# Kernel optimization log

Hardware: AMD Instinct MI355X
Metric: run time of the kernel (lower is better)

The kernel has to match this reference:

```python
import jax, jax.numpy as jnp
import numpy as np

N = 100000          # nodes
E = 1600000         # edges
IN, H, E1, E2, K = 256, 128, 128, 128, 3


def setup_inputs() -> dict:
    key = jax.random.key(0)
    ks = jax.random.split(key, 8)
    s = 0.02
    return {
        "x": jax.random.normal(ks[0], (N, IN), dtype=jnp.float32),
        "edge_index": jax.random.randint(ks[1], (2, E), 0, N),
        "edge_weight": jax.random.uniform(ks[2], (E,), dtype=jnp.float32),
        "W1": jax.random.normal(ks[3], (IN, H), dtype=jnp.float32) * s,
        "b1": jnp.zeros((H,), jnp.float32),
        "cheb1_W": jax.random.normal(ks[4], (K, H, E1), dtype=jnp.float32) * s,
        "cheb1_b": jnp.zeros((E1,), jnp.float32),
        "cheb2_W": jax.random.normal(ks[5], (K, E1, E2), dtype=jnp.float32) * s,
        "cheb2_b": jnp.zeros((E2,), jnp.float32),
        "W2": jax.random.normal(ks[6], (E2, 2), dtype=jnp.float32) * s,
        "b2": jnp.zeros((2,), jnp.float32),
    }


def _cheb_conv(x, row, col, wn, Ws, b):
    """PyG ChebConv with sym normalization, lambda_max=2.
    Scaled Laplacian L_hat = L_sym - I = -D^{-1/2} A D^{-1/2} (zero diagonal),
    so L_hat @ v is a single gather/scale/scatter over edges.
    Tx_0 = x; Tx_1 = L_hat x; Tx_k = 2 L_hat Tx_{k-1} - Tx_{k-2}.
    """
    n = x.shape[0]

    def Lx(v):
        return jax.ops.segment_sum(-wn[:, None] * v[col], row, num_segments=n)

    Tx0 = x
    out = Tx0 @ Ws[0]
    Tx1 = Lx(Tx0)
    out = out + Tx1 @ Ws[1]
    for k in range(2, Ws.shape[0]):
        Tx2 = 2.0 * Lx(Tx1) - Tx0
        out = out + Tx2 @ Ws[k]
        Tx0, Tx1 = Tx1, Tx2
    return out + b


def reference(x, edge_index, edge_weight, W1, b1, cheb1_W, cheb1_b,
              cheb2_W, cheb2_b, W2, b2):
    row, col = edge_index[0], edge_index[1]
    n = x.shape[0]
    # symmetric normalization of edge weights (shared by both convs)
    deg = jax.ops.segment_sum(edge_weight, row, num_segments=n)
    safe = jnp.where(deg > 0, deg, 1.0)
    dinv = jnp.where(deg > 0, jax.lax.rsqrt(safe), 0.0)
    wn = dinv[row] * edge_weight * dinv[col]

    # dropout is identity in eval mode
    h = jax.nn.relu(x @ W1 + b1)
    h = jax.nn.relu(_cheb_conv(h, row, col, wn, cheb1_W, cheb1_b))
    h = jax.nn.relu(_cheb_conv(h, row, col, wn, cheb2_W, cheb2_b))
    logits = h @ W2 + b2
    return jax.nn.softmax(logits, axis=1)
```

## Files before the change

kernel.cpp:

```cpp
#include <hip/hip_runtime.h>
#include <hip/hip_bf16.h>
#include <stdint.h>

typedef __bf16 bf16_t;
typedef __bf16 bf16x8 __attribute__((ext_vector_type(8)));
typedef float f32x4 __attribute__((ext_vector_type(4)));
typedef float f32x2 __attribute__((ext_vector_type(2)));
typedef float floatv4 __attribute__((ext_vector_type(4)));

static __device__ __forceinline__ void gload16(const void* g, void* l){
  __builtin_amdgcn_global_load_lds((const __attribute__((address_space(1))) void*)g,
                                   (__attribute__((address_space(3))) void*)l, 16, 0, 0);
}
static __device__ __forceinline__ void acc4_fp8(float* a, unsigned w, float wt){
  f32x2 lo, hi;
  unsigned wh = w >> 16;
  asm("v_cvt_pk_f32_fp8 %0, %1" : "=v"(lo) : "v"(w));
  asm("v_cvt_pk_f32_fp8 %0, %1" : "=v"(hi) : "v"(wh));
  a[0] += wt*lo[0]; a[1] += wt*lo[1]; a[2] += wt*hi[0]; a[3] += wt*hi[1];
}
static __device__ __forceinline__ void dec4_fp8(float* d, unsigned w){
  f32x2 lo, hi;
  unsigned wh = w >> 16;
  asm("v_cvt_pk_f32_fp8 %0, %1" : "=v"(lo) : "v"(w));
  asm("v_cvt_pk_f32_fp8 %0, %1" : "=v"(hi) : "v"(wh));
  d[0] = lo[0]; d[1] = lo[1]; d[2] = hi[0]; d[3] = hi[1];
}
static __device__ __forceinline__ unsigned cvt2fp8(float a, float b){
  unsigned r;
  asm("v_cvt_pk_fp8_f32 %0, %1, %2" : "=v"(r) : "v"(a), "v"(b));
  return r & 0xffffu;
}
static __device__ __forceinline__ uint8_t cvt1fp8(float a){
  unsigned r;
  asm("v_cvt_pk_fp8_f32 %0, %1, %1" : "=v"(r) : "v"(a));
  return (uint8_t)r;
}
static __device__ __forceinline__ unsigned packEdge(int col, float w_pos){
  unsigned b = __float_as_uint(w_pos) + 0x8000u;
  return ((b >> 16) << 17) | (unsigned)col;
}
static __device__ __forceinline__ float edgeWpos(unsigned u){
  return __uint_as_float((u >> 17) << 16);
}
static __device__ __forceinline__ float edgeWneg(unsigned u){
  return __uint_as_float(0x80000000u | ((u >> 17) << 16));
}

constexpr int NN = 100000;
constexpr int NE = 1600000;
constexpr int NB_G  = (NN + 127)/128;
constexpr int NBIN = (NN + 127)/128;
constexpr int EPB  = 4096;
constexpr int NBB  = (NE + EPB - 1)/EPB;
constexpr int MAXBE = 3072;
constexpr int NB_TW8 = (2*3*128*128)/256;

__global__ __launch_bounds__(256) void k_scanbins(const int* __restrict__ bincnt,
                                                  int* __restrict__ binptr,
                                                  int* __restrict__ rowptr){
  __shared__ int s[256];
  int t = threadIdx.x;
  int b0 = t*4;
  int c[4]; int tot = 0;
  #pragma unroll
  for (int j = 0; j < 4; ++j){
    int b = b0 + j;
    c[j] = (b < NBIN) ? bincnt[b] : 0;
    tot += c[j];
  }
  s[t] = tot;
  __syncthreads();
  for (int off = 1; off < 256; off <<= 1){
    int v = (t >= off) ? s[t - off] : 0;
    __syncthreads();
    s[t] += v;
    __syncthreads();
  }
  int ex = s[t] - tot;
  #pragma unroll
  for (int j = 0; j < 4; ++j){
    int b = b0 + j;
    if (b < NBIN) binptr[b] = ex;
    ex += c[j];
  }
  if (t == 255){ binptr[NBIN] = ex; rowptr[NN] = ex; }
}

__global__ __launch_bounds__(256) void k_binB(const int* __restrict__ row,
                                              const int* __restrict__ col,
                                              const float* __restrict__ w,
                                              const int* __restrict__ binptr,
                                              const int* __restrict__ blockbase,
                                              int2* __restrict__ temp){
  __shared__ int h[NBIN];
  for (int b = threadIdx.x; b < NBIN; b += 256) h[b] = 0;
  __syncthreads();
  int base = blockIdx.x * EPB;
  for (int k = 0; k < EPB; k += 256){
    int i = base + k + threadIdx.x;
    if (i < NE){
      int r = row[i];
      int b = r >> 7;
      int rank = atomicAdd(&h[b], 1);
      int pos = binptr[b] + blockbase[blockIdx.x * NBIN + b] + rank;
      temp[pos] = make_int2(col[i] | ((r & 127) << 17), __float_as_int(w[i]));
    }
  }
}

__global__ __launch_bounds__(256) void k_binC(const int2* __restrict__ temp,
                                              const int* __restrict__ binptr,
                                              unsigned* __restrict__ ec,
                                              int* __restrict__ rowptr,
                                              float* __restrict__ dinv, int n){
  __shared__ int2 sbuf[MAXBE];
  __shared__ int cnt[128];
  __shared__ int scan[128];
  __shared__ int estart[128];
  const int b = blockIdx.x;
  const int e0 = binptr[b];
  int nb = binptr[b+1] - e0; if (nb > MAXBE) nb = MAXBE;
  const int t = threadIdx.x;
  if (t < 128) cnt[t] = 0;
  __syncthreads();
  for (int k = t; k < nb; k += 256)
    atomicAdd(&cnt[(temp[e0+k].x >> 17) & 127], 1);
  __syncthreads();
  if (t < 128) scan[t] = cnt[t];
  __syncthreads();
  for (int off = 1; off < 128; off <<= 1){
    int v = (t < 128 && t >= off) ? scan[t - off] : 0;
    __syncthreads();
    if (t < 128) scan[t] += v;
    __syncthreads();
  }
  if (t < 128){ estart[t] = scan[t] - cnt[t]; cnt[t] = 0; }
  __syncthreads();
  for (int k = t; k < nb; k += 256){
    int2 q = temp[e0+k];
    int rl = (q.x >> 17) & 127;
    int rank = atomicAdd(&cnt[rl], 1);
    sbuf[estart[rl] + rank] = q;
  }
  __syncthreads();
  for (int k = t; k < nb; k += 256){
    int2 q = sbuf[k];
    ec[e0 + k] = packEdge(q.x & 0x1FFFF, __int_as_float(q.y));
  }
  if (t < 128){
    int gid = b*128 + t;
    if (gid < n){
      rowptr[gid] = e0 + estart[t];
      float s = 0.f;
      int s0 = estart[t], c = cnt[t];
      for (int j = 0; j < c; ++j) s += __int_as_float(sbuf[s0+j].y);
      dinv[gid] = (s > 0.f) ? rsqrtf(s) : 0.f;
    }
  }
}

__global__ __launch_bounds__(256) void k_norm(unsigned* __restrict__ ec,
                                              const int* __restrict__ rowptr,
                                              const float* __restrict__ dinv, int n){
  int node = blockIdx.x*4 + (threadIdx.x >> 6);
  if (node >= n) return;
  int lane = threadIdx.x & 63;
  int e0 = rowptr[node], e1 = rowptr[node+1];
  float dr = dinv[node];
  for (int e = e0 + lane; e < e1; e += 64){
    unsigned u = ec[e];
    int c = u & 0x1FFFF;
    float wn = dr * edgeWpos(u) * dinv[c];
    ec[e] = packEdge(c, wn);
  }
}

__global__ void k_transw1(const float* __restrict__ W1, bf16_t* __restrict__ Wt1){
  int idx = blockIdx.x*256 + threadIdx.x;
  int c = idx >> 14, r = (idx >> 7) & 127, j = idx & 127;
  Wt1[(c << 14) + (j << 7) + r] = (bf16_t)W1[idx];
}

__global__ __launch_bounds__(256) void k_gemm1_fused(
    const float* __restrict__ x, const bf16_t* __restrict__ Wt, const float* __restrict__ bias,
    uint8_t* __restrict__ out8, int M,
    const int* __restrict__ row, int* __restrict__ bincnt, int* __restrict__ blockbase,
    const float* __restrict__ c1W, const float* __restrict__ c2W,
    uint8_t* __restrict__ W8c1, uint8_t* __restrict__ W8c2)
{
  __shared__ uint8_t lds[2][16384];
  __shared__ int hA[NBIN];
  const int tid = threadIdx.x;

  if (blockIdx.x >= NB_G + NBB){
    int base = (blockIdx.x - NB_G - NBB)*256 + tid;
    int m = base / 49152;
    int local = base - m*49152;
    const float* src = m ? c2W : c1W;
    uint8_t* dst = m ? W8c2 : W8c1;
    int c = local >> 14, r = (local >> 7) & 127, j = local & 127;
    dst[(c << 14) + (j << 7) + r] = cvt1fp8(src[local]);
    return;
  }
  if (blockIdx.x >= NB_G){
    int bb = blockIdx.x - NB_G;
    for (int b = tid; b < NBIN; b += 256) hA[b] = 0;
    __syncthreads();
    int base = bb * EPB;
    for (int k = 0; k < EPB; k += 256){
      int i = base + k + tid;
      if (i < NE) atomicAdd(&hA[row[i] >> 7], 1);
    }
    __syncthreads();
    for (int b = tid; b < NBIN; b += 256){
      int c = hA[b];
      blockbase[bb * NBIN + b] = c ? atomicAdd(&bincnt[b], c) : 0;
    }
    return;
  }

  const int wave = tid >> 6, lane = tid & 63;
  const int wm = wave >> 1, wn = wave & 1;
  const int l15 = lane & 15, lq = lane >> 4;
  const int blockRow = blockIdx.x * 128;
  const int strow = tid >> 3;
  const int scell = tid & 7;

  f32x4 acc[4][4];
  #pragma unroll
  for (int a = 0; a < 4; ++a)
    #pragma unroll
    for (int b = 0; b < 4; ++b) acc[a][b] = f32x4{0.f,0.f,0.f,0.f};

  #pragma unroll
  for (int j = 0; j < 4; ++j){
    int r = j*32 + strow;
    int gr = blockRow + r; if (gr > M-1) gr = M-1;
    gload16((const char*)x + (size_t)gr*1024 + ((scell ^ (r&7)) << 4),
            &lds[0][j*4096 + tid*16]);
  }

  #pragma unroll
  for (int s = 0; s < 8; ++s){
    if (s < 7){
      #pragma unroll
      for (int j = 0; j < 4; ++j){
        int r = j*32 + strow;
        int gr = blockRow + r; if (gr > M-1) gr = M-1;
        gload16((const char*)x + (size_t)gr*1024 + (s+1)*128 + ((scell ^ (r&7)) << 4),
                &lds[(s+1)&1][j*4096 + tid*16]);
      }
    }
    __syncthreads();
    const uint8_t* buf = lds[s&1];
    bf16x8 af[4], bfr[4];
    #pragma unroll
    for (int fm = 0; fm < 4; ++fm){
      int r = wm*64 + fm*16 + l15;
      floatv4 v0 = *(const floatv4*)(buf + r*128 + (((lq*2    ) ^ (r&7)) << 4));
      floatv4 v1 = *(const floatv4*)(buf + r*128 + (((lq*2 + 1) ^ (r&7)) << 4));
      bf16x8 t;
      t[0]=(bf16_t)v0[0]; t[1]=(bf16_t)v0[1]; t[2]=(bf16_t)v0[2]; t[3]=(bf16_t)v0[3];
      t[4]=(bf16_t)v1[0]; t[5]=(bf16_t)v1[1]; t[6]=(bf16_t)v1[2]; t[7]=(bf16_t)v1[3];
      af[fm] = t;
    }
    #pragma unroll
    for (int fn = 0; fn < 4; ++fn)
      bfr[fn] = *(const bf16x8*)(Wt + ((size_t)(((s>>2) << 7) + wn*64 + fn*16 + l15) << 7) + (s&3)*32 + lq*8);
    #pragma unroll
    for (int fm = 0; fm < 4; ++fm)
      #pragma unroll
      for (int fn = 0; fn < 4; ++fn)
        acc[fm][fn] = __builtin_amdgcn_mfma_f32_16x16x32_bf16(af[fm], bfr[fn], acc[fm][fn], 0, 0, 0);
    __syncthreads();
  }
  #pragma unroll
  for (int fm = 0; fm < 4; ++fm){
    #pragma unroll
    for (int j = 0; j < 4; ++j){
      int growo = blockRow + wm*64 + fm*16 + lq*4 + j;
      if (growo < M){
        #pragma unroll
        for (int fn = 0; fn < 4; ++fn){
          int c = wn*64 + fn*16 + l15;
          float v = fmaxf(acc[fm][fn][j] + bias[c], 0.f);
          out8[((size_t)growo << 7) + c] = cvt1fp8(v);
        }
      }
    }
  }
}

__global__ __launch_bounds__(256) void k_gemm8(
    const uint8_t* __restrict__ a0, const uint8_t* __restrict__ a1, const uint8_t* __restrict__ a2,
    const uint8_t* __restrict__ Wt8, const float* __restrict__ bias,
    uint8_t* __restrict__ out8,
    const float* __restrict__ W2h, const float* __restrict__ b2h, float* __restrict__ outh,
    int M)
{
  __shared__ uint8_t lds[2][8192];
  __shared__ float logits[128][2][2];
  const int tid = threadIdx.x;
  const int wave = tid >> 6, lane = tid & 63;
  const int wm = wave >> 1, wn = wave & 1;
  const int l15 = lane & 15, lq = lane >> 4;
  const int blockRow = blockIdx.x * 128;

  f32x4 acc[4][4];
  #pragma unroll
  for (int a = 0; a < 4; ++a)
    #pragma unroll
    for (int b = 0; b < 4; ++b) acc[a][b] = f32x4{0.f,0.f,0.f,0.f};

  #pragma unroll
  for (int j = 0; j < 2; ++j){
    int flat = j*256 + tid;
    int r = flat >> 2, cell = flat & 3;
    int gr = blockRow + r; if (gr > M-1) gr = M-1;
    gload16(a0 + (size_t)gr*128 + ((cell ^ ((r>>1)&3)) << 4), &lds[0][flat << 4]);
  }

  #pragma unroll
  for (int s = 0; s < 6; ++s){
    if (s < 5){
      const int sn = s + 1;
      const uint8_t* srcn = (sn>>1) == 0 ? a0 : ((sn>>1) == 1 ? a1 : a2);
      #pragma unroll
      for (int j = 0; j < 2; ++j){
        int flat = j*256 + tid;
        int r = flat >> 2, cell = flat & 3;
        int gr = blockRow + r; if (gr > M-1) gr = M-1;
        gload16(srcn + (size_t)gr*128 + (sn&1)*64 + ((cell ^ ((r>>1)&3)) << 4),
                &lds[sn&1][flat << 4]);
      }
    }
    __syncthreads();
    const uint8_t* buf = lds[s&1];
    #pragma unroll
    for (int kk32 = 0; kk32 < 2; ++kk32){
      long af[4], bfr[4];
      #pragma unroll
      for (int fm = 0; fm < 4; ++fm){
        int r = wm*64 + fm*16 + l15;
        int cell = kk32*2 + (lq >> 1);
        af[fm] = *(const long*)(buf + r*64 + ((cell ^ ((r>>1)&3)) << 4) + (lq & 1)*8);
      }
      #pragma unroll
      for (int fn = 0; fn < 4; ++fn)
        bfr[fn] = *(const long*)(Wt8 + ((size_t)(((s>>1) << 7) + wn*64 + fn*16 + l15) << 7)
                                 + (s&1)*64 + kk32*32 + lq*8);
      #pragma unroll
      for (int fm = 0; fm < 4; ++fm)
        #pragma unroll
        for (int fn = 0; fn < 4; ++fn)
          acc[fm][fn] = __builtin_amdgcn_mfma_f32_16x16x32_fp8_fp8(af[fm], bfr[fn], acc[fm][fn], 0, 0, 0);
    }
    __syncthreads();
  }

  if (outh){
    float w2l[8];
    #pragma unroll
    for (int fn = 0; fn < 4; ++fn){
      int c = wn*64 + fn*16 + l15;
      w2l[fn*2]   = W2h[c*2];
      w2l[fn*2+1] = W2h[c*2+1];
    }
    #pragma unroll
    for (int fm = 0; fm < 4; ++fm){
      #pragma unroll
      for (int j = 0; j < 4; ++j){
        int r = wm*64 + fm*16 + lq*4 + j;
        float p0 = 0.f, p1 = 0.f;
        #pragma unroll
        for (int fn = 0; fn < 4; ++fn){
          float v = fmaxf(acc[fm][fn][j] + bias[wn*64 + fn*16 + l15], 0.f);
          p0 += v*w2l[fn*2];
          p1 += v*w2l[fn*2+1];
        }
        #pragma unroll
        for (int m = 1; m < 16; m <<= 1){
          p0 += __shfl_xor(p0, m, 64);
          p1 += __shfl_xor(p1, m, 64);
        }
        if (l15 == 0){
          logits[r][wn][0] = p0;
          logits[r][wn][1] = p1;
        }
      }
    }
    __syncthreads();
    if (tid < 128){
      int node = blockRow + tid;
      if (node < M){
        float l0 = logits[tid][0][0] + logits[tid][1][0] + b2h[0];
        float l1 = logits[tid][0][1] + logits[tid][1][1] + b2h[1];
        float mx = fmaxf(l0, l1);
        float e0 = __expf(l0 - mx), e1 = __expf(l1 - mx);
        float inv = 1.f / (e0 + e1);
        *(float2*)(outh + (size_t)node*2) = make_float2(e0*inv, e1*inv);
      }
    }
  } else {
    #pragma unroll
    for (int fm = 0; fm < 4; ++fm){
      #pragma unroll
      for (int j = 0; j < 4; ++j){
        int growo = blockRow + wm*64 + fm*16 + lq*4 + j;
        if (growo < M){
          #pragma unroll
          for (int fn = 0; fn < 4; ++fn){
            int c = wn*64 + fn*16 + l15;
            float v = fmaxf(acc[fm][fn][j] + bias[c], 0.f);
            out8[((size_t)growo << 7) + c] = cvt1fp8(v);
          }
        }
      }
    }
  }
}

__global__ __launch_bounds__(256) void k_spmm8(
    const int* __restrict__ rowptr, const unsigned* __restrict__ ec,
    const uint8_t* __restrict__ V8, const uint8_t* __restrict__ sub8, float alpha,
    uint8_t* __restrict__ out8, int n)
{
  const int lane = threadIdx.x & 63;
  const int wave = threadIdx.x >> 6;
  const int g = lane >> 4;
  const int s = lane & 15;
  const int node = blockIdx.x*16 + wave*4 + g;
  if (node >= n) return;

  int e = rowptr[node];
  const int e1 = rowptr[node+1];
  const int fb = s << 3;

  float acc[8] = {0.f,0.f,0.f,0.f,0.f,0.f,0.f,0.f};

  for (; e + 8 <= e1; e += 8){
    unsigned u0 = ec[e],   u1 = ec[e+1], u2 = ec[e+2], u3 = ec[e+3];
    unsigned u4 = ec[e+4], u5 = ec[e+5], u6 = ec[e+6], u7 = ec[e+7];
    uint2 p0 = *(const uint2*)(V8 + (((size_t)(u0 & 0x1FFFF)) << 7) + fb);
    uint2 p1 = *(const uint2*)(V8 + (((size_t)(u1 & 0x1FFFF)) << 7) + fb);
    uint2 p2 = *(const uint2*)(V8 + (((size_t)(u2 & 0x1FFFF)) << 7) + fb);
    uint2 p3 = *(const uint2*)(V8 + (((size_t)(u3 & 0x1FFFF)) << 7) + fb);
    uint2 p4 = *(const uint2*)(V8 + (((size_t)(u4 & 0x1FFFF)) << 7) + fb);
    uint2 p5 = *(const uint2*)(V8 + (((size_t)(u5 & 0x1FFFF)) << 7) + fb);
    uint2 p6 = *(const uint2*)(V8 + (((size_t)(u6 & 0x1FFFF)) << 7) + fb);
    uint2 p7 = *(const uint2*)(V8 + (((size_t)(u7 & 0x1FFFF)) << 7) + fb);
    float w0 = edgeWneg(u0), w1 = edgeWneg(u1), w2 = edgeWneg(u2), w3 = edgeWneg(u3);
    float w4 = edgeWneg(u4), w5 = edgeWneg(u5), w6 = edgeWneg(u6), w7 = edgeWneg(u7);
    acc4_fp8(acc,   p0.x, w0); acc4_fp8(acc+4, p0.y, w0);
    acc4_fp8(acc,   p1.x, w1); acc4_fp8(acc+4, p1.y, w1);
    acc4_fp8(acc,   p2.x, w2); acc4_fp8(acc+4, p2.y, w2);
    acc4_fp8(acc,   p3.x, w3); acc4_fp8(acc+4, p3.y, w3);
    acc4_fp8(acc,   p4.x, w4); acc4_fp8(acc+4, p4.y, w4);
    acc4_fp8(acc,   p5.x, w5); acc4_fp8(acc+4, p5.y, w5);
    acc4_fp8(acc,   p6.x, w6); acc4_fp8(acc+4, p6.y, w6);
    acc4_fp8(acc,   p7.x, w7); acc4_fp8(acc+4, p7.y, w7);
  }
  for (; e + 4 <= e1; e += 4){
    unsigned u0 = ec[e], u1 = ec[e+1], u2 = ec[e+2], u3 = ec[e+3];
    uint2 p0 = *(const uint2*)(V8 + (((size_t)(u0 & 0x1FFFF)) << 7) + fb);
    uint2 p1 = *(const uint2*)(V8 + (((size_t)(u1 & 0x1FFFF)) << 7) + fb);
    uint2 p2 = *(const uint2*)(V8 + (((size_t)(u2 & 0x1FFFF)) << 7) + fb);
    uint2 p3 = *(const uint2*)(V8 + (((size_t)(u3 & 0x1FFFF)) << 7) + fb);
    float w0 = edgeWneg(u0), w1 = edgeWneg(u1), w2 = edgeWneg(u2), w3 = edgeWneg(u3);
    acc4_fp8(acc,   p0.x, w0); acc4_fp8(acc+4, p0.y, w0);
    acc4_fp8(acc,   p1.x, w1); acc4_fp8(acc+4, p1.y, w1);
    acc4_fp8(acc,   p2.x, w2); acc4_fp8(acc+4, p2.y, w2);
    acc4_fp8(acc,   p3.x, w3); acc4_fp8(acc+4, p3.y, w3);
  }
  for (; e < e1; ++e){
    unsigned u = ec[e];
    uint2 p = *(const uint2*)(V8 + (((size_t)(u & 0x1FFFF)) << 7) + fb);
    float w = edgeWneg(u);
    acc4_fp8(acc, p.x, w); acc4_fp8(acc+4, p.y, w);
  }

  float r[8];
  #pragma unroll
  for (int i = 0; i < 8; ++i) r[i] = alpha*acc[i];
  if (sub8){
    uint2 sv = *(const uint2*)(sub8 + (((size_t)node) << 7) + fb);
    float sd[8];
    dec4_fp8(sd,     sv.x);
    dec4_fp8(sd + 4, sv.y);
    #pragma unroll
    for (int i = 0; i < 8; ++i) r[i] -= sd[i];
  }
  uint2 o8;
  o8.x = cvt2fp8(r[0], r[1]) | (cvt2fp8(r[2], r[3]) << 16);
  o8.y = cvt2fp8(r[4], r[5]) | (cvt2fp8(r[6], r[7]) << 16);
  *(uint2*)(out8 + (((size_t)node) << 7) + fb) = o8;
}


extern "C" void kernel_launch(void* const* d_in, const int* in_sizes, int n_in,
                              void* d_out, int out_size, void* d_ws, size_t ws_size,
                              hipStream_t stream)
{
  const float* x   = (const float*)d_in[0];
  const int*   ei  = (const int*)d_in[1];
  const float* ew  = (const float*)d_in[2];
  const float* W1  = (const float*)d_in[3];
  const float* b1  = (const float*)d_in[4];
  const float* c1W = (const float*)d_in[5];
  const float* c1b = (const float*)d_in[6];
  const float* c2W = (const float*)d_in[7];
  const float* c2b = (const float*)d_in[8];
  const float* W2  = (const float*)d_in[9];
  const float* b2  = (const float*)d_in[10];
  float* out = (float*)d_out;

  const int n = NN, e = NE;
  const int* row = ei;
  const int* col = ei + e;

  char* ws = (char*)d_ws;
  size_t off = 0;
  auto carve = [&](size_t bytes)->void*{
    void* p = ws + off;
    off += (bytes + 255) & ~(size_t)255;
    return p;
  };
  uint8_t* q8a = (uint8_t*)carve((size_t)n*128);
  uint8_t* B8  = (uint8_t*)carve((size_t)n*128);
  uint8_t* C8  = (uint8_t*)carve((size_t)n*128);
  uint8_t* D8  = (uint8_t*)carve((size_t)n*128);
  float*  dinv = (float*)carve((size_t)n*4);
  int*    rowptr = (int*)carve((size_t)(n+1)*4);
  unsigned* ec = (unsigned*)carve((size_t)e*4);
  int*    bincnt = (int*)carve((size_t)NBIN*4);
  int*    binptr = (int*)carve((size_t)(NBIN+1)*4);
  int*    blockbase = (int*)carve((size_t)NBB*NBIN*4);
  bf16_t*  Wt1  = (bf16_t*)carve(2*128*128*2);
  uint8_t* W8c1 = (uint8_t*)carve(3*128*128);
  uint8_t* W8c2 = (uint8_t*)carve(3*128*128);
  int2* temp = (int2*)D8;
  (void)ws_size; (void)in_sizes; (void)n_in; (void)out_size;

  const int NB_W = (n + 3)/4;
  const int NB_S = (n + 15)/16;

  hipMemsetAsync(bincnt, 0, (size_t)NBIN*4, stream);
  k_transw1<<<128,256,0,stream>>>(W1, Wt1);
  k_gemm1_fused<<<NB_G + NBB + NB_TW8,256,0,stream>>>(
      x, Wt1, b1, q8a, n, row, bincnt, blockbase, c1W, c2W, W8c1, W8c2);
  k_scanbins<<<1,256,0,stream>>>(bincnt, binptr, rowptr);
  k_binB<<<NBB,256,0,stream>>>(row, col, ew, binptr, blockbase, temp);
  k_binC<<<NBIN,256,0,stream>>>(temp, binptr, ec, rowptr, dinv, n);
  k_norm<<<NB_W,256,0,stream>>>(ec, rowptr, dinv, n);

  k_spmm8<<<NB_S,256,0,stream>>>(rowptr, ec, q8a, nullptr, 1.f, B8, n);
  k_spmm8<<<NB_S,256,0,stream>>>(rowptr, ec, B8, q8a, 2.f, C8, n);
  k_gemm8<<<NB_G,256,0,stream>>>(q8a, B8, C8, W8c1, c1b, D8, nullptr, nullptr, nullptr, n);
  k_spmm8<<<NB_S,256,0,stream>>>(rowptr, ec, D8, nullptr, 1.f, B8, n);
  k_spmm8<<<NB_S,256,0,stream>>>(rowptr, ec, B8, D8, 2.f, C8, n);
  k_gemm8<<<NB_G,256,0,stream>>>(D8, B8, C8, W8c2, c2b, nullptr, W2, b2, out, n);
}
```

Measured before the change: 305.6 us.

## Reschedule CSR build phases and fuse edge normalization into first SpMM

The bin-count histogram and the W1 transpose are merged into one kernel launched before the GEMM. The scatter phase (old binB) now runs inside the fused GEMM launch, so the edge scatter overlaps with the dense GEMM. The separate normalization pass is removed. The first SpMM computes normalized weights on the fly and writes them back into the edge array for later passes. This cuts two launches and one full pass over the edges, at the cost of extra dinv gathers in the first SpMM.

New measurement: 295.2 us. 1.04x faster.

```diff
diff --git a/kernel.cpp b/kernel.cpp
--- a/kernel.cpp
+++ b/kernel.cpp
@@ -55,6 +55,34 @@
 constexpr int NBB  = (NE + EPB - 1)/EPB;
 constexpr int MAXBE = 3072;
 constexpr int NB_TW8 = (2*3*128*128)/256;
+constexpr int NB_TW1 = (2*128*128)/256;
+
+__global__ __launch_bounds__(256) void k_binA_tw(const int* __restrict__ row,
+                                                 int* __restrict__ bincnt,
+                                                 int* __restrict__ blockbase,
+                                                 const float* __restrict__ W1,
+                                                 bf16_t* __restrict__ Wt1){
+  __shared__ int h[NBIN];
+  const int tid = threadIdx.x;
+  if (blockIdx.x >= NBB){
+    int idx = (blockIdx.x - NBB)*256 + tid;
+    int c = idx >> 14, r = (idx >> 7) & 127, j = idx & 127;
+    Wt1[(c << 14) + (j << 7) + r] = (bf16_t)W1[idx];
+    return;
+  }
+  for (int b = tid; b < NBIN; b += 256) h[b] = 0;
+  __syncthreads();
+  int base = blockIdx.x * EPB;
+  for (int k = 0; k < EPB; k += 256){
+    int i = base + k + tid;
+    if (i < NE) atomicAdd(&h[row[i] >> 7], 1);
+  }
+  __syncthreads();
+  for (int b = tid; b < NBIN; b += 256){
+    int c = h[b];
+    blockbase[blockIdx.x * NBIN + b] = c ? atomicAdd(&bincnt[b], c) : 0;
+  }
+}
 
 __global__ __launch_bounds__(256) void k_scanbins(const int* __restrict__ bincnt,
                                                   int* __restrict__ binptr,
@@ -85,28 +113,6 @@
     ex += c[j];
   }
   if (t == 255){ binptr[NBIN] = ex; rowptr[NN] = ex; }
-}
-
-__global__ __launch_bounds__(256) void k_binB(const int* __restrict__ row,
-                                              const int* __restrict__ col,
-                                              const float* __restrict__ w,
-                                              const int* __restrict__ binptr,
-                                              const int* __restrict__ blockbase,
-                                              int2* __restrict__ temp){
-  __shared__ int h[NBIN];
-  for (int b = threadIdx.x; b < NBIN; b += 256) h[b] = 0;
-  __syncthreads();
-  int base = blockIdx.x * EPB;
-  for (int k = 0; k < EPB; k += 256){
-    int i = base + k + threadIdx.x;
-    if (i < NE){
-      int r = row[i];
-      int b = r >> 7;
-      int rank = atomicAdd(&h[b], 1);
-      int pos = binptr[b] + blockbase[blockIdx.x * NBIN + b] + rank;
-      temp[pos] = make_int2(col[i] | ((r & 127) << 17), __float_as_int(w[i]));
-    }
-  }
 }
 
 __global__ __launch_bounds__(256) void k_binC(const int2* __restrict__ temp,
@@ -160,37 +166,16 @@
   }
 }
 
-__global__ __launch_bounds__(256) void k_norm(unsigned* __restrict__ ec,
-                                              const int* __restrict__ rowptr,
-                                              const float* __restrict__ dinv, int n){
-  int node = blockIdx.x*4 + (threadIdx.x >> 6);
-  if (node >= n) return;
-  int lane = threadIdx.x & 63;
-  int e0 = rowptr[node], e1 = rowptr[node+1];
-  float dr = dinv[node];
-  for (int e = e0 + lane; e < e1; e += 64){
-    unsigned u = ec[e];
-    int c = u & 0x1FFFF;
-    float wn = dr * edgeWpos(u) * dinv[c];
-    ec[e] = packEdge(c, wn);
-  }
-}
-
-__global__ void k_transw1(const float* __restrict__ W1, bf16_t* __restrict__ Wt1){
-  int idx = blockIdx.x*256 + threadIdx.x;
-  int c = idx >> 14, r = (idx >> 7) & 127, j = idx & 127;
-  Wt1[(c << 14) + (j << 7) + r] = (bf16_t)W1[idx];
-}
-
 __global__ __launch_bounds__(256) void k_gemm1_fused(
     const float* __restrict__ x, const bf16_t* __restrict__ Wt, const float* __restrict__ bias,
     uint8_t* __restrict__ out8, int M,
-    const int* __restrict__ row, int* __restrict__ bincnt, int* __restrict__ blockbase,
+    const int* __restrict__ row, const int* __restrict__ col, const float* __restrict__ w,
+    const int* __restrict__ binptr, const int* __restrict__ blockbase, int2* __restrict__ temp,
     const float* __restrict__ c1W, const float* __restrict__ c2W,
     uint8_t* __restrict__ W8c1, uint8_t* __restrict__ W8c2)
 {
   __shared__ uint8_t lds[2][16384];
-  __shared__ int hA[NBIN];
+  __shared__ int hB[NBIN];
   const int tid = threadIdx.x;
 
   if (blockIdx.x >= NB_G + NBB){
@@ -205,17 +190,18 @@
   }
   if (blockIdx.x >= NB_G){
     int bb = blockIdx.x - NB_G;
-    for (int b = tid; b < NBIN; b += 256) hA[b] = 0;
+    for (int b = tid; b < NBIN; b += 256) hB[b] = 0;
     __syncthreads();
     int base = bb * EPB;
     for (int k = 0; k < EPB; k += 256){
       int i = base + k + tid;
-      if (i < NE) atomicAdd(&hA[row[i] >> 7], 1);
-    }
-    __syncthreads();
-    for (int b = tid; b < NBIN; b += 256){
-      int c = hA[b];
-      blockbase[bb * NBIN + b] = c ? atomicAdd(&bincnt[b], c) : 0;
+      if (i < NE){
+        int r = row[i];
+        int b = r >> 7;
+        int rank = atomicAdd(&hB[b], 1);
+        int pos = binptr[b] + blockbase[bb * NBIN + b] + rank;
+        temp[pos] = make_int2(col[i] | ((r & 127) << 17), __float_as_int(w[i]));
+      }
     }
     return;
   }
@@ -419,6 +405,62 @@
       }
     }
   }
+}
+
+__global__ __launch_bounds__(256) void k_spmm8n(
+    const int* __restrict__ rowptr, unsigned* __restrict__ ec,
+    const float* __restrict__ dinv,
+    const uint8_t* __restrict__ V8, uint8_t* __restrict__ out8, int n)
+{
+  const int lane = threadIdx.x & 63;
+  const int wave = threadIdx.x >> 6;
+  const int g = lane >> 4;
+  const int s = lane & 15;
+  const int node = blockIdx.x*16 + wave*4 + g;
+  if (node >= n) return;
+
+  int e = rowptr[node];
+  const int e1 = rowptr[node+1];
+  const int fb = s << 3;
+  const float dr = dinv[node];
+
+  float acc[8] = {0.f,0.f,0.f,0.f,0.f,0.f,0.f,0.f};
+
+  for (; e + 4 <= e1; e += 4){
+    unsigned u0 = ec[e], u1 = ec[e+1], u2 = ec[e+2], u3 = ec[e+3];
+    int c0 = u0 & 0x1FFFF, c1 = u1 & 0x1FFFF, c2 = u2 & 0x1FFFF, c3 = u3 & 0x1FFFF;
+    uint2 p0 = *(const uint2*)(V8 + (((size_t)c0) << 7) + fb);
+    uint2 p1 = *(const uint2*)(V8 + (((size_t)c1) << 7) + fb);
+    uint2 p2 = *(const uint2*)(V8 + (((size_t)c2) << 7) + fb);
+    uint2 p3 = *(const uint2*)(V8 + (((size_t)c3) << 7) + fb);
+    float wn0 = dr * edgeWpos(u0) * dinv[c0];
+    float wn1 = dr * edgeWpos(u1) * dinv[c1];
+    float wn2 = dr * edgeWpos(u2) * dinv[c2];
+    float wn3 = dr * edgeWpos(u3) * dinv[c3];
+    if (s == 0){
+      ec[e]   = packEdge(c0, wn0);
+      ec[e+1] = packEdge(c1, wn1);
+      ec[e+2] = packEdge(c2, wn2);
+      ec[e+3] = packEdge(c3, wn3);
+    }
+    acc4_fp8(acc, p0.x, -wn0); acc4_fp8(acc+4, p0.y, -wn0);
+    acc4_fp8(acc, p1.x, -wn1); acc4_fp8(acc+4, p1.y, -wn1);
+    acc4_fp8(acc, p2.x, -wn2); acc4_fp8(acc+4, p2.y, -wn2);
+    acc4_fp8(acc, p3.x, -wn3); acc4_fp8(acc+4, p3.y, -wn3);
+  }
+  for (; e < e1; ++e){
+    unsigned u = ec[e];
+    int c = u & 0x1FFFF;
+    uint2 p = *(const uint2*)(V8 + (((size_t)c) << 7) + fb);
+    float wn = dr * edgeWpos(u) * dinv[c];
+    if (s == 0) ec[e] = packEdge(c, wn);
+    acc4_fp8(acc, p.x, -wn); acc4_fp8(acc+4, p.y, -wn);
+  }
+
+  uint2 o8;
+  o8.x = cvt2fp8(acc[0], acc[1]) | (cvt2fp8(acc[2], acc[3]) << 16);
+  o8.y = cvt2fp8(acc[4], acc[5]) | (cvt2fp8(acc[6], acc[7]) << 16);
+  *(uint2*)(out8 + (((size_t)node) << 7) + fb) = o8;
 }
 
 __global__ __launch_bounds__(256) void k_spmm8(
@@ -542,19 +584,16 @@
   int2* temp = (int2*)D8;
   (void)ws_size; (void)in_sizes; (void)n_in; (void)out_size;
 
-  const int NB_W = (n + 3)/4;
   const int NB_S = (n + 15)/16;
 
   hipMemsetAsync(bincnt, 0, (size_t)NBIN*4, stream);
-  k_transw1<<<128,256,0,stream>>>(W1, Wt1);
+  k_binA_tw<<<NBB + NB_TW1,256,0,stream>>>(row, bincnt, blockbase, W1, Wt1);
+  k_scanbins<<<1,256,0,stream>>>(bincnt, binptr, rowptr);
   k_gemm1_fused<<<NB_G + NBB + NB_TW8,256,0,stream>>>(
-      x, Wt1, b1, q8a, n, row, bincnt, blockbase, c1W, c2W, W8c1, W8c2);
-  k_scanbins<<<1,256,0,stream>>>(bincnt, binptr, rowptr);
-  k_binB<<<NBB,256,0,stream>>>(row, col, ew, binptr, blockbase, temp);
+      x, Wt1, b1, q8a, n, row, col, ew, binptr, blockbase, temp, c1W, c2W, W8c1, W8c2);
   k_binC<<<NBIN,256,0,stream>>>(temp, binptr, ec, rowptr, dinv, n);
-  k_norm<<<NB_W,256,0,stream>>>(ec, rowptr, dinv, n);
-
-  k_spmm8<<<NB_S,256,0,stream>>>(rowptr, ec, q8a, nullptr, 1.f, B8, n);
+
+  k_spmm8n<<<NB_S,256,0,stream>>>(rowptr, ec, dinv, q8a, B8, n);
   k_spmm8<<<NB_S,256,0,stream>>>(rowptr, ec, B8, q8a, 2.f, C8, n);
   k_gemm8<<<NB_G,256,0,stream>>>(q8a, B8, C8, W8c1, c1b, D8, nullptr, nullptr, nullptr, n);
   k_spmm8<<<NB_S,256,0,stream>>>(rowptr, ec, D8, nullptr, 1.f, B8, n);
```
